# Kernel optimization log

Hardware: AMD Instinct MI355X
Metric: run time of the kernel (lower is better)

Reference implementation:

```python
import jax, jax.numpy as jnp
import numpy as np

TOL = 5            # proximity_tolerance
DECAY = 0.8        # distance_decay
SWITCH_W = 20.0    # switch_loss_weight


def setup_inputs() -> dict:
    key = jax.random.key(0)
    k1, k2 = jax.random.split(key)
    B, S, C = 512, 8192, 4
    logits = jax.random.normal(k1, (B, S, C), dtype=jnp.float32)
    labels = jax.random.randint(k2, (B, S), 0, 4, dtype=jnp.int32)
    class_weights = jnp.array([1.0, 1.0, SWITCH_W, SWITCH_W], dtype=jnp.float32)
    return {"logits": logits, "labels": labels, "class_weights": class_weights}


def _nearest_dist(mask):
    """Per row: distance from each position to the nearest True in `mask`.
    Returns a large value (> S) where the row has no True. mask: [B, S] bool."""
    B, S = mask.shape
    idx = jnp.arange(S, dtype=jnp.int32)
    big = jnp.int32(4 * S)
    # index of nearest True at-or-before each position (forward cummax)
    prev = jax.lax.cummax(jnp.where(mask, idx, -big), axis=1)
    # index of nearest True at-or-after each position (backward cummin)
    nxt = jnp.flip(jax.lax.cummin(jnp.flip(jnp.where(mask, idx, 3 * big), axis=1), axis=1), axis=1)
    return jnp.minimum(idx - prev, nxt - idx)  # [B, S] int32


def reference(logits, labels, class_weights):
    B, S, C = logits.shape
    safe = jnp.where(labels < 0, 0, labels)  # handle ignore_index=-100
    logp = jax.nn.log_softmax(logits, axis=-1)
    nll = -jnp.take_along_axis(logp, safe[..., None], axis=-1)[..., 0]
    # torch F.cross_entropy(weight=w, reduction='none'): weight[y] * nll, 0 at ignore_index
    ce = jnp.where(labels < 0, 0.0, nll * class_weights[safe])  # [B, S]

    preds = jnp.argmax(logits, axis=-1)

    for c in (2, 3):  # switch-to-auto, switch-to-allo
        tmask = labels == c
        pmask = preds == c
        # predicted switches near (0 < d <= tol) a true switch of same type -> decay
        d_pt = _nearest_dist(tmask)  # dist to nearest true switch (big if none)
        near = (d_pt > 0) & (d_pt <= TOL)
        decay = jnp.where(pmask & near,
                          DECAY ** jnp.minimum(d_pt, TOL).astype(jnp.float32),
                          1.0)
        # true switches: x2 if no predicted switch of this type in the row,
        # x1.5 if nearest predicted switch is farther than tol
        d_tp = _nearest_dist(pmask)  # dist to nearest predicted switch
        any_pred = jnp.any(pmask, axis=1, keepdims=True)
        tfac = jnp.where(tmask,
                         jnp.where(any_pred,
                                   jnp.where(d_tp > TOL, 1.5, 1.0),
                                   2.0),
                         1.0)
        ce = ce * decay * tfac

    valid = (labels >= 0).astype(jnp.float32)
    return (ce * valid).sum() / jnp.maximum(valid.sum(), 1.0)
```

## Files before the change

kernel.cpp:

```cpp
#include <hip/hip_runtime.h>


#define S_LEN 8192
#define NTHREADS 1024
#define NITER (S_LEN / NTHREADS)
#define NWORDS (S_LEN / 32)
#define NWAVES (NTHREADS / 64)

#if __has_builtin(__builtin_amdgcn_exp2f)
#define HW_EXP2(x) __builtin_amdgcn_exp2f(x)
#else
#define HW_EXP2(x) exp2f(x)
#endif
#if __has_builtin(__builtin_amdgcn_logf)
#define HW_LOG2(x) __builtin_amdgcn_logf(x)
#else
#define HW_LOG2(x) log2f(x)
#endif

__device__ inline float prox_factor(unsigned tw, unsigned pw, bool anyp) {
    bool tm = (tw >> 5) & 1u;
    bool pm = (pw >> 5) & 1u;
    float f = 1.0f;
    unsigned tn = tw & ~(1u << 5);
    if (pm && !tm && tn) {
        if      (tn & 0x050u) f = 0.8f;
        else if (tn & 0x088u) f = 0.64f;
        else if (tn & 0x104u) f = 0.512f;
        else if (tn & 0x202u) f = 0.4096f;
        else                  f = 0.32768f;
    }
    if (tm) {
        f *= anyp ? (pw ? 1.0f : 1.5f) : 2.0f;
    }
    return f;
}

__device__ inline unsigned w11(unsigned lo, unsigned hi, int off) {
    unsigned long long c = (unsigned long long)lo | ((unsigned long long)hi << 32);
    return (unsigned)((c >> off) & 0x7FFull);
}

__global__ __launch_bounds__(NTHREADS)
void prox_loss_main(const float* __restrict__ logits,
                    const int* __restrict__ labels,
                    const float* __restrict__ cw,
                    float* __restrict__ acc) {
    __shared__ unsigned t2g[NWORDS + 2], t3g[NWORDS + 2];
    __shared__ unsigned p2g[NWORDS + 2], p3g[NWORDS + 2];
    __shared__ unsigned anyf[2];
    __shared__ float part_s[NWAVES], part_v[NWAVES];

    const int tid = threadIdx.x;
    const long base = (long)blockIdx.x * S_LEN;
    const float4* __restrict__ lg4 = reinterpret_cast<const float4*>(logits);

    if (tid == 0) { t2g[0] = 0u; t3g[0] = 0u; p2g[0] = 0u; p3g[0] = 0u; }
    if (tid == 1) {
        t2g[NWORDS + 1] = 0u; t3g[NWORDS + 1] = 0u;
        p2g[NWORDS + 1] = 0u; p3g[NWORDS + 1] = 0u;
    }
    if (tid < 2) anyf[tid] = 0u;

    const float w0 = cw[0], w1 = cw[1], w2 = cw[2], w3 = cw[3];
    const float L2E = 1.4426950408889634f;
    const float LN2 = 0.6931471805599453f;

    float ce_reg[NITER];
    float local_valid = 0.0f;

#pragma unroll
    for (int k = 0; k < NITER; ++k) {
        const int pos = k * NTHREADS + tid;
        const long g = base + pos;
        const float4 x = lg4[g];
        const int lab = labels[g];

        const bool pr2 = (x.z > x.x) && (x.z > x.y) && (x.w <= x.z);
        const bool pr3 = (x.w > x.x) && (x.w > x.y) && (x.w > x.z);

        const float s = HW_EXP2(x.x * L2E) + HW_EXP2(x.y * L2E)
                      + HW_EXP2(x.z * L2E) + HW_EXP2(x.w * L2E);
        const float lse = HW_LOG2(s) * LN2;

        const int safe = (lab < 0) ? 0 : lab;
        const bool b0 = (safe & 1) != 0;
        const bool b1 = (safe & 2) != 0;
        const float xy = b0 ? x.y : x.x;
        const float zw = b0 ? x.w : x.z;
        const float xl = b1 ? zw : xy;
        const float wy = b0 ? w1 : w0;
        const float wz = b0 ? w3 : w2;
        const float ws = b1 ? wz : wy;
        ce_reg[k] = (lab < 0) ? 0.0f : ws * (lse - xl);
        local_valid += (lab >= 0) ? 1.0f : 0.0f;

        const unsigned long long bt2 = __ballot(lab == 2);
        const unsigned long long bt3 = __ballot(lab == 3);
        const unsigned long long bp2 = __ballot(pr2);
        const unsigned long long bp3 = __ballot(pr3);
        if ((tid & 63) == 0) {
            const int widx = (pos >> 5) + 1;
            t2g[widx] = (unsigned)bt2; t2g[widx + 1] = (unsigned)(bt2 >> 32);
            t3g[widx] = (unsigned)bt3; t3g[widx + 1] = (unsigned)(bt3 >> 32);
            p2g[widx] = (unsigned)bp2; p2g[widx + 1] = (unsigned)(bp2 >> 32);
            p3g[widx] = (unsigned)bp3; p3g[widx + 1] = (unsigned)(bp3 >> 32);
        }
    }
    __syncthreads();

    if (tid < NWORDS) {
        if (p2g[tid + 1] != 0u) atomicOr(&anyf[0], 1u);
        if (p3g[tid + 1] != 0u) atomicOr(&anyf[1], 1u);
    }
    __syncthreads();
    const bool any2 = anyf[0] != 0u;
    const bool any3 = anyf[1] != 0u;

    float local_sum = 0.0f;
#pragma unroll
    for (int k = 0; k < NITER; ++k) {
        const int pos = k * NTHREADS + tid;
        const int bse = pos - 5;
        const int j = (bse >> 5) + 1;
        const int off = bse & 31;
        const unsigned tw2 = w11(t2g[j], t2g[j + 1], off);
        const unsigned pw2 = w11(p2g[j], p2g[j + 1], off);
        const unsigned tw3 = w11(t3g[j], t3g[j + 1], off);
        const unsigned pw3 = w11(p3g[j], p3g[j + 1], off);
        float f = ce_reg[k];
        f *= prox_factor(tw2, pw2, any2);
        f *= prox_factor(tw3, pw3, any3);
        local_sum += f;
    }

    for (int o = 32; o > 0; o >>= 1) {
        local_sum   += __shfl_down(local_sum, o);
        local_valid += __shfl_down(local_valid, o);
    }
    const int wv = tid >> 6;
    if ((tid & 63) == 0) { part_s[wv] = local_sum; part_v[wv] = local_valid; }
    __syncthreads();

    if (tid == 0) {
        float ssum = 0.0f, vsum = 0.0f;
        for (int i = 0; i < NWAVES; ++i) { ssum += part_s[i]; vsum += part_v[i]; }
        atomicAdd(&acc[0], ssum);
        atomicAdd(&acc[1], vsum);
    }
}

__global__ void prox_loss_finalize(const float* __restrict__ acc,
                                   float* __restrict__ out) {
    out[0] = acc[0] / fmaxf(acc[1], 1.0f);
}

extern "C" void kernel_launch(void* const* d_in, const int* in_sizes, int n_in,
                              void* d_out, int out_size, void* d_ws, size_t ws_size,
                              hipStream_t stream) {
    const float* logits = (const float*)d_in[0];
    const int*   labels = (const int*)d_in[1];
    const float* cw     = (const float*)d_in[2];
    float* out = (float*)d_out;
    float* acc = (float*)d_ws;

    const int B = in_sizes[1] / S_LEN;

    hipMemsetAsync(acc, 0, 2 * sizeof(float), stream);
    prox_loss_main<<<B, NTHREADS, 0, stream>>>(logits, labels, cw, acc);
    prox_loss_finalize<<<1, 1, 0, stream>>>(acc, out);
}
```

Before: 116.5 us.

## Prefetch all loads upfront, drop memset and atomics, reduce per-wave partials in finalize

All eight float4 logit loads and label loads per thread are issued before any compute, so more memory requests are in flight. The shared-memory atomicOr pass for the any-prediction flags, and its extra barrier, are replaced by per-wave flags OR'd together after the one barrier. The block-level reduction and global atomics become per-wave float2 partials written to the workspace and summed by a 1024-thread finalize kernel, which removes the memset launch. This raises register pressure in the main kernel and makes the finalize kernel do more work.

```diff
diff --git a/kernel.cpp b/kernel.cpp
--- a/kernel.cpp
+++ b/kernel.cpp
@@ -45,11 +45,10 @@
 void prox_loss_main(const float* __restrict__ logits,
                     const int* __restrict__ labels,
                     const float* __restrict__ cw,
-                    float* __restrict__ acc) {
+                    float2* __restrict__ ws) {
     __shared__ unsigned t2g[NWORDS + 2], t3g[NWORDS + 2];
     __shared__ unsigned p2g[NWORDS + 2], p3g[NWORDS + 2];
-    __shared__ unsigned anyf[2];
-    __shared__ float part_s[NWAVES], part_v[NWAVES];
+    __shared__ unsigned wany[NWAVES];
 
     const int tid = threadIdx.x;
     const long base = (long)blockIdx.x * S_LEN;
@@ -60,45 +59,53 @@
         t2g[NWORDS + 1] = 0u; t3g[NWORDS + 1] = 0u;
         p2g[NWORDS + 1] = 0u; p3g[NWORDS + 1] = 0u;
     }
-    if (tid < 2) anyf[tid] = 0u;
 
     const float w0 = cw[0], w1 = cw[1], w2 = cw[2], w3 = cw[3];
     const float L2E = 1.4426950408889634f;
     const float LN2 = 0.6931471805599453f;
 
+    float4 x[NITER]; int lv[NITER];
+#pragma unroll
+    for (int k = 0; k < NITER; ++k) {
+        const long g = base + (long)k * NTHREADS + tid;
+        x[k] = lg4[g];
+        lv[k] = labels[g];
+    }
+
     float ce_reg[NITER];
     float local_valid = 0.0f;
+    unsigned myany = 0u;
 
 #pragma unroll
     for (int k = 0; k < NITER; ++k) {
         const int pos = k * NTHREADS + tid;
-        const long g = base + pos;
-        const float4 x = lg4[g];
-        const int lab = labels[g];
+        const float4 v = x[k];
+        const int lab = lv[k];
 
-        const bool pr2 = (x.z > x.x) && (x.z > x.y) && (x.w <= x.z);
-        const bool pr3 = (x.w > x.x) && (x.w > x.y) && (x.w > x.z);
+        const bool pr2 = (v.z > v.x) && (v.z > v.y) && (v.w <= v.z);
+        const bool pr3 = (v.w > v.x) && (v.w > v.y) && (v.w > v.z);
 
-        const float s = HW_EXP2(x.x * L2E) + HW_EXP2(x.y * L2E)
-                      + HW_EXP2(x.z * L2E) + HW_EXP2(x.w * L2E);
+        const float s = HW_EXP2(v.x * L2E) + HW_EXP2(v.y * L2E)
+                      + HW_EXP2(v.z * L2E) + HW_EXP2(v.w * L2E);
         const float lse = HW_LOG2(s) * LN2;
 
         const int safe = (lab < 0) ? 0 : lab;
         const bool b0 = (safe & 1) != 0;
         const bool b1 = (safe & 2) != 0;
-        const float xy = b0 ? x.y : x.x;
-        const float zw = b0 ? x.w : x.z;
+        const float xy = b0 ? v.y : v.x;
+        const float zw = b0 ? v.w : v.z;
         const float xl = b1 ? zw : xy;
         const float wy = b0 ? w1 : w0;
         const float wz = b0 ? w3 : w2;
-        const float ws = b1 ? wz : wy;
-        ce_reg[k] = (lab < 0) ? 0.0f : ws * (lse - xl);
+        const float wsc = b1 ? wz : wy;
+        ce_reg[k] = (lab < 0) ? 0.0f : wsc * (lse - xl);
         local_valid += (lab >= 0) ? 1.0f : 0.0f;
 
         const unsigned long long bt2 = __ballot(lab == 2);
         const unsigned long long bt3 = __ballot(lab == 3);
         const unsigned long long bp2 = __ballot(pr2);
         const unsigned long long bp3 = __ballot(pr3);
+        myany |= (bp2 != 0ull ? 1u : 0u) | (bp3 != 0ull ? 2u : 0u);
         if ((tid & 63) == 0) {
             const int widx = (pos >> 5) + 1;
             t2g[widx] = (unsigned)bt2; t2g[widx + 1] = (unsigned)(bt2 >> 32);
@@ -107,15 +114,15 @@
             p3g[widx] = (unsigned)bp3; p3g[widx + 1] = (unsigned)(bp3 >> 32);
         }
     }
+    if ((tid & 63) == 0) wany[tid >> 6] = myany;
+
     __syncthreads();
 
-    if (tid < NWORDS) {
-        if (p2g[tid + 1] != 0u) atomicOr(&anyf[0], 1u);
-        if (p3g[tid + 1] != 0u) atomicOr(&anyf[1], 1u);
-    }
-    __syncthreads();
-    const bool any2 = anyf[0] != 0u;
-    const bool any3 = anyf[1] != 0u;
+    unsigned aw = 0u;
+#pragma unroll
+    for (int i = 0; i < NWAVES; ++i) aw |= wany[i];
+    const bool any2 = (aw & 1u) != 0u;
+    const bool any3 = (aw & 2u) != 0u;
 
     float local_sum = 0.0f;
 #pragma unroll
@@ -138,21 +145,34 @@
         local_sum   += __shfl_down(local_sum, o);
         local_valid += __shfl_down(local_valid, o);
     }
-    const int wv = tid >> 6;
-    if ((tid & 63) == 0) { part_s[wv] = local_sum; part_v[wv] = local_valid; }
-    __syncthreads();
-
-    if (tid == 0) {
-        float ssum = 0.0f, vsum = 0.0f;
-        for (int i = 0; i < NWAVES; ++i) { ssum += part_s[i]; vsum += part_v[i]; }
-        atomicAdd(&acc[0], ssum);
-        atomicAdd(&acc[1], vsum);
+    if ((tid & 63) == 0) {
+        ws[(long)blockIdx.x * NWAVES + (tid >> 6)] =
+            make_float2(local_sum, local_valid);
     }
 }
 
-__global__ void prox_loss_finalize(const float* __restrict__ acc,
-                                   float* __restrict__ out) {
-    out[0] = acc[0] / fmaxf(acc[1], 1.0f);
+__global__ __launch_bounds__(1024)
+void prox_loss_finalize(const float2* __restrict__ ws,
+                        float* __restrict__ out,
+                        int nslots) {
+    __shared__ float ps[16], pv[16];
+    const int tid = threadIdx.x;
+    float s = 0.0f, v = 0.0f;
+    for (int i = tid; i < nslots; i += 1024) {
+        const float2 t = ws[i];
+        s += t.x; v += t.y;
+    }
+    for (int o = 32; o > 0; o >>= 1) {
+        s += __shfl_down(s, o);
+        v += __shfl_down(v, o);
+    }
+    if ((tid & 63) == 0) { ps[tid >> 6] = s; pv[tid >> 6] = v; }
+    __syncthreads();
+    if (tid == 0) {
+        float S = 0.0f, V = 0.0f;
+        for (int i = 0; i < 16; ++i) { S += ps[i]; V += pv[i]; }
+        out[0] = S / fmaxf(V, 1.0f);
+    }
 }
 
 extern "C" void kernel_launch(void* const* d_in, const int* in_sizes, int n_in,
@@ -162,11 +182,10 @@
     const int*   labels = (const int*)d_in[1];
     const float* cw     = (const float*)d_in[2];
     float* out = (float*)d_out;
-    float* acc = (float*)d_ws;
+    float2* ws = (float2*)d_ws;
 
     const int B = in_sizes[1] / S_LEN;
 
-    hipMemsetAsync(acc, 0, 2 * sizeof(float), stream);
-    prox_loss_main<<<B, NTHREADS, 0, stream>>>(logits, labels, cw, acc);
-    prox_loss_finalize<<<1, 1, 0, stream>>>(acc, out);
+    prox_loss_main<<<B, NTHREADS, 0, stream>>>(logits, labels, cw, ws);
+    prox_loss_finalize<<<1, 1024, 0, stream>>>(ws, out, B * NWAVES);
 }
```

After: 111.7 us. 4.1% less time.
